# Optimization experiments

Measured on AMD Instinct MI355X. Metric: run time of the kernel, lower is better.

Reference implementation:

```python
import jax, jax.numpy as jnp
import numpy as np

N_NODES = 50000
N_EDGES = 1600000
N_GRAPHS = 512
IN_SIZE = 44
HIDDEN = 256
CONV_NUMS = 3


def setup_inputs() -> dict:
    key = jax.random.key(0)
    ks = jax.random.split(key, 10)
    h = jax.random.normal(ks[0], (N_NODES, IN_SIZE), dtype=jnp.float32)
    src = jax.random.randint(ks[1], (N_EDGES,), 0, N_NODES)
    dst = jax.random.randint(ks[2], (N_EDGES,), 0, N_NODES)
    graph_ids = jnp.sort(jax.random.randint(ks[3], (N_NODES,), 0, N_GRAPHS))
    # learned params (kaiming-ish scale)
    W_proj = jax.random.normal(ks[4], (IN_SIZE, HIDDEN), dtype=jnp.float32) * (2.0 / IN_SIZE) ** 0.5
    b_proj = jnp.zeros((HIDDEN,), dtype=jnp.float32)
    W_lin = jax.random.normal(ks[5], (HIDDEN, HIDDEN), dtype=jnp.float32) * (2.0 / HIDDEN) ** 0.5
    b_lin = jnp.zeros((HIDDEN,), dtype=jnp.float32)
    W_out = jax.random.normal(ks[6], (HIDDEN * CONV_NUMS, HIDDEN), dtype=jnp.float32) * (2.0 / (HIDDEN * CONV_NUMS)) ** 0.5
    b_out = jnp.zeros((HIDDEN,), dtype=jnp.float32)
    return {"h": h, "src": src, "dst": dst, "graph_ids": graph_ids,
            "W_proj": W_proj, "b_proj": b_proj, "W_lin": W_lin, "b_lin": b_lin,
            "W_out": W_out, "b_out": b_out}


def reference(h, src, dst, graph_ids, W_proj, b_proj, W_lin, b_lin, W_out, b_out):
    # initial projection
    h = h @ W_proj + b_proj  # [N, HIDDEN]
    # in-degree for mean aggregation (nodes with 0 in-edges get 0 aggregate)
    ones_e = jnp.ones((src.shape[0],), dtype=h.dtype)
    deg = jax.ops.segment_sum(ones_e, dst, num_segments=N_NODES)  # [N]
    inv_deg = jnp.where(deg > 0, 1.0 / jnp.maximum(deg, 1.0), 0.0)[:, None]
    outs = []
    for _ in range(CONV_NUMS):
        # DGL GINConv(mean, eps=0): h' = linear(h + mean_{u in N(v)} h_u)
        agg = jax.ops.segment_sum(h[src], dst, num_segments=N_NODES) * inv_deg
        h = (h + agg) @ W_lin + b_lin  # shared linear across layers
        outs.append(h)
    res = jnp.concatenate(outs, axis=1) @ W_out + b_out  # [N, HIDDEN]
    # dgl.mean_nodes: per-graph mean readout
    cnt = jax.ops.segment_sum(jnp.ones((N_NODES,), dtype=res.dtype), graph_ids, num_segments=N_GRAPHS)
    g_sum = jax.ops.segment_sum(res, graph_ids, num_segments=N_GRAPHS)
    return g_sum / jnp.maximum(cnt, 1.0)[:, None]
```

## Files before the change

kernel.cpp:

```cpp
#include <hip/hip_runtime.h>
#include <hip/hip_fp8.h>

#define N_NODES   50000
#define N_EDGES   1600000
#define N_GRAPHS  512
#define IN_SIZE   44
#define HIDDEN    256
#define CONV_NUMS 3
#define NBK       ((N_NODES + 255) / 256)
#define XK        48
#define XK8       64

typedef __attribute__((ext_vector_type(8))) short short8v;
typedef __attribute__((ext_vector_type(4))) float f32x4;
typedef __attribute__((ext_vector_type(2))) float f32x2;

__device__ __forceinline__ float bf2f(unsigned short u) {
    return __uint_as_float(((unsigned int)u) << 16);
}
__device__ __forceinline__ unsigned short f2bf(float f) {
    unsigned int u = __float_as_uint(f);
    unsigned int r = (u + 0x7fffu + ((u >> 16) & 1u)) >> 16;
    return (unsigned short)r;
}

#if __has_builtin(__builtin_amdgcn_cvt_f32_fp8)
template <int SEL>
__device__ __forceinline__ float fp8tof(unsigned int w) {
    return __builtin_amdgcn_cvt_f32_fp8((int)w, SEL);
}
#else
template <int SEL>
__device__ __forceinline__ float fp8tof(unsigned int w) {
    __hip_fp8_e4m3 q;
    q.__x = (__hip_fp8_storage_t)((w >> (SEL * 8)) & 0xff);
    return (float)q;
}
#endif

#if __has_builtin(__builtin_amdgcn_cvt_pk_f32_fp8)
template <int HI>
__device__ __forceinline__ f32x2 pk2f(unsigned int w) {
    return __builtin_amdgcn_cvt_pk_f32_fp8((int)w, HI != 0);
}
#else
template <int HI>
__device__ __forceinline__ f32x2 pk2f(unsigned int w) {
    f32x2 r;
    r.x = fp8tof<2 * HI>(w);
    r.y = fp8tof<2 * HI + 1>(w);
    return r;
}
#endif

#if __has_builtin(__builtin_amdgcn_cvt_pk_fp8_f32)
__device__ __forceinline__ unsigned int pk4fp8(float f0, float f1, float f2, float f3) {
    int lo = __builtin_amdgcn_cvt_pk_fp8_f32(f0, f1, 0, false);
    return (unsigned int)__builtin_amdgcn_cvt_pk_fp8_f32(f2, f3, lo, true);
}
#else
__device__ __forceinline__ unsigned int pk4fp8(float f0, float f1, float f2, float f3) {
    __hip_fp8_e4m3 a(f0), b(f1), c(f2), d(f3);
    return (unsigned int)a.__x | ((unsigned int)b.__x << 8) |
           ((unsigned int)c.__x << 16) | ((unsigned int)d.__x << 24);
}
#endif

__device__ __forceinline__ unsigned char f2fp8(float f) {
    return (unsigned char)(pk4fp8(f, 0.f, 0.f, 0.f) & 0xff);
}

__global__ __launch_bounds__(256) void k_build0(const int* __restrict__ dst,
                                                const int* __restrict__ gid,
                                                const float* __restrict__ Wl,
                                                const float* __restrict__ Wproj,
                                                const float* __restrict__ X,
                                                int* __restrict__ bucket_cnt,
                                                int* __restrict__ gcnt,
                                                unsigned short* __restrict__ WlPack,
                                                unsigned short* __restrict__ WprojPack,
                                                unsigned short* __restrict__ Xb,
                                                unsigned char* __restrict__ Xb8p) {
    int b = blockIdx.x;
    int tid = threadIdx.x;
    if (b < 512) {
        __shared__ int hb[NBK];
        __shared__ int hg[N_GRAPHS];
        for (int i = tid; i < NBK; i += 256) hb[i] = 0;
        for (int i = tid; i < N_GRAPHS; i += 256) hg[i] = 0;
        __syncthreads();
        int t = b * 256 + tid;
        int stride = 512 * 256;
        for (int e = t; e < N_EDGES; e += stride) atomicAdd(&hb[dst[e] >> 8], 1);
        for (int v = t; v < N_NODES; v += stride) atomicAdd(&hg[gid[v]], 1);
        __syncthreads();
        for (int i = tid; i < NBK; i += 256) if (hb[i]) atomicAdd(&bucket_cnt[i], hb[i]);
        for (int i = tid; i < N_GRAPHS; i += 256) if (hg[i]) atomicAdd(&gcnt[i], hg[i]);
    } else if (b < 544) {
        int i = (b - 512) * 256 + tid;
        int kg = i >> 8, n = i & 255;
        short8v v;
#pragma unroll
        for (int j = 0; j < 8; j++) v[j] = (short)f2bf(Wl[(kg * 8 + j) * HIDDEN + n]);
        *(short8v*)(WlPack + (size_t)(kg * 256 + n) * 8) = v;
    } else if (b < 552) {
        int i = (b - 544) * 256 + tid;
        int kg = i >> 8, n = i & 255;
        short8v v;
#pragma unroll
        for (int j = 0; j < 8; j++) {
            int k = kg * 8 + j;
            v[j] = (k < IN_SIZE) ? (short)f2bf(Wproj[k * HIDDEN + n]) : (short)0;
        }
        *(short8v*)(WprojPack + (size_t)(kg * 256 + n) * 8) = v;
    } else {
        const int TOT8 = N_NODES * XK8;
        int id0 = (b - 552) * 2048 + tid;
#pragma unroll
        for (int j = 0; j < 8; j++) {
            int id = id0 + j * 256;
            if (id < TOT8) {
                int row = id >> 6, c = id & 63;
                float val = (c < IN_SIZE) ? X[row * IN_SIZE + c] : 0.f;
                Xb8p[id] = f2fp8(val);
                if (c < XK) Xb[(size_t)row * XK + c] = f2bf(val);
            }
        }
    }
}

__global__ void k_bscan(const int* __restrict__ bucket_cnt, int* __restrict__ bucket_base,
                        int* __restrict__ bucket_cursor, int* __restrict__ row_ptr) {
    __shared__ int s[256];
    int t = threadIdx.x;
    int v = (t < NBK) ? bucket_cnt[t] : 0;
    s[t] = v;
    __syncthreads();
    for (int off = 1; off < 256; off <<= 1) {
        int a = (t >= off) ? s[t - off] : 0;
        __syncthreads();
        s[t] += a;
        __syncthreads();
    }
    if (t < NBK) {
        int base = s[t] - v;
        bucket_base[t] = base;
        bucket_cursor[t] = base;
    }
    if (t == 0) {
        bucket_base[NBK] = N_EDGES;
        row_ptr[N_NODES] = N_EDGES;
    }
}

#define BCH 8192
__global__ __launch_bounds__(256) void k_passB(const int* __restrict__ src,
                                               const int* __restrict__ dst,
                                               int* __restrict__ bucket_cursor,
                                               int* __restrict__ pairs) {
    __shared__ int hist[NBK];
    __shared__ int excl[NBK];
    __shared__ int cur[NBK];
    __shared__ int gbase[NBK];
    __shared__ int lp[BCH];
    __shared__ int sc[256];
    int tid = threadIdx.x;
    int e0 = blockIdx.x * BCH;
    int cnt = min(BCH, N_EDGES - e0);
    for (int i = tid; i < NBK; i += 256) hist[i] = 0;
    __syncthreads();
    for (int i = tid; i < cnt; i += 256) atomicAdd(&hist[dst[e0 + i] >> 8], 1);
    __syncthreads();
    int hv = (tid < NBK) ? hist[tid] : 0;
    sc[tid] = hv;
    __syncthreads();
    for (int off = 1; off < 256; off <<= 1) {
        int a = (tid >= off) ? sc[tid - off] : 0;
        __syncthreads();
        sc[tid] += a;
        __syncthreads();
    }
    if (tid < NBK) {
        excl[tid] = sc[tid] - hv;
        cur[tid]  = sc[tid] - hv;
    }
    __syncthreads();
    for (int i = tid; i < cnt; i += 256) {
        int d = dst[e0 + i];
        int b = d >> 8;
        int pos = atomicAdd(&cur[b], 1);
        lp[pos] = (b << 24) | ((d & 255) << 16) | src[e0 + i];
    }
    __syncthreads();
    if (tid < NBK && hist[tid] > 0)
        gbase[tid] = atomicAdd(&bucket_cursor[tid], hist[tid]);
    __syncthreads();
    for (int i = tid; i < cnt; i += 256) {
        int p = lp[i];
        int b = (p >> 24) & 0xff;
        pairs[gbase[b] + (i - excl[b])] = p;
    }
}

__global__ __launch_bounds__(256) void k_passC(const int* __restrict__ pairs,
                                               const int* __restrict__ bucket_base,
                                               int* __restrict__ row_ptr,
                                               unsigned short* __restrict__ colu) {
    __shared__ int hist[256];
    __shared__ int cur[256];
    __shared__ int sc[256];
    int b = blockIdx.x;
    int tid = threadIdx.x;
    int v0 = b << 8;
    int e0 = bucket_base[b], e1 = bucket_base[b + 1];
    hist[tid] = 0;
    __syncthreads();
    for (int i = e0 + tid; i < e1; i += 256) atomicAdd(&hist[(pairs[i] >> 16) & 0xff], 1);
    __syncthreads();
    int hv = hist[tid];
    sc[tid] = hv;
    __syncthreads();
    for (int off = 1; off < 256; off <<= 1) {
        int a = (tid >= off) ? sc[tid - off] : 0;
        __syncthreads();
        sc[tid] += a;
        __syncthreads();
    }
    int base = e0 + sc[tid] - hv;
    int v = v0 + tid;
    if (v < N_NODES) row_ptr[v] = base;
    cur[tid] = base;
    __syncthreads();
    for (int i = e0 + tid; i < e1; i += 256) {
        int p = pairs[i];
        int pos = atomicAdd(&cur[(p >> 16) & 0xff], 1);
        colu[pos] = (unsigned short)(p & 0xffff);
    }
}

#define TLS 264
#define K1S 72
__global__ __launch_bounds__(512, 8) void k_layer1(const unsigned short* __restrict__ Xb,
                                                   const unsigned char* __restrict__ Xb8p,
                                                   const int* __restrict__ row_ptr,
                                                   const unsigned short* __restrict__ colu,
                                                   const unsigned short* __restrict__ WprojPack,
                                                   const float* __restrict__ bp,
                                                   const unsigned short* __restrict__ WlPack,
                                                   const float* __restrict__ bl,
                                                   const int* __restrict__ gid,
                                                   unsigned short* __restrict__ hout,
                                                   unsigned char* __restrict__ hout8,
                                                   float* __restrict__ GsumL) {
    __shared__ unsigned short tl[64 * TLS];
    unsigned short* tl1 = tl;
    float* redbase = (float*)(tl + 64 * K1S);
    __shared__ float bpm[64];
    __shared__ int gl[64];
    int tid = threadIdx.x;
    int w = tid >> 6, lane = tid & 63, quad = lane >> 4, l16 = lane & 15;
    int g = lane >> 4, sub = lane & 15;
    int m0 = blockIdx.x * 64;
    float* red = redbase + w * 256;

    const unsigned int* X8 = (const unsigned int*)Xb8p;
    for (int rr = 0; rr < 8; rr++) {
        int r = w * 8 + rr;
        int v = m0 + r;
        f32x2 A = {0.f, 0.f};
        f32x2 Bv = {0.f, 0.f};
        int s = 0, e = 0;
        if (v < N_NODES) { s = row_ptr[v]; e = row_ptr[v + 1]; }
        int i = s;
        for (; i + 8 <= e; i += 8) {
            int ua = colu[i + g];
            int ub = colu[i + 4 + g];
            unsigned int pa = X8[ua * 16 + sub];
            unsigned int pb = X8[ub * 16 + sub];
            A  += pk2f<0>(pa) + pk2f<0>(pb);
            Bv += pk2f<1>(pa) + pk2f<1>(pb);
        }
        if (i + 4 <= e) {
            int ua = colu[i + g];
            unsigned int pa = X8[ua * 16 + sub];
            A += pk2f<0>(pa);
            Bv += pk2f<1>(pa);
            i += 4;
        }
        if (i + g < e) {
            int ua = colu[i + g];
            unsigned int pa = X8[ua * 16 + sub];
            A += pk2f<0>(pa);
            Bv += pk2f<1>(pa);
        }
        *(f32x4*)(red + g * 64 + sub * 4) = (f32x4){A.x, A.y, Bv.x, Bv.y};
        float ssum = (red[0 * 64 + lane] + red[1 * 64 + lane])
                   + (red[2 * 64 + lane] + red[3 * 64 + lane]);
        float val = 0.f;
        float mul = 1.f;
        if (v < N_NODES) {
            float inv = 0.f;
            if (e > s) { inv = 1.0f / (float)(e - s); mul = 2.f; }
            float self = (lane < XK) ? bf2f(Xb[(size_t)v * XK + lane]) : 0.f;
            val = self + inv * ssum;
        }
        tl1[r * K1S + lane] = (lane < XK) ? f2bf(val) : (unsigned short)0;
        if (lane == 0) bpm[r] = mul;
    }
    if (tid < 64) gl[tid] = (m0 + tid < N_NODES) ? gid[m0 + tid] : -1;
    __syncthreads();

    int n0 = w * 32;
    f32x4 acc[4][2];
#pragma unroll
    for (int mt = 0; mt < 4; mt++) {
        acc[mt][0] = (f32x4){0.f, 0.f, 0.f, 0.f};
        acc[mt][1] = (f32x4){0.f, 0.f, 0.f, 0.f};
    }
#pragma unroll
    for (int ks = 0; ks < 2; ks++) {
        int kg = ks * 4 + quad;
        short8v bfr0 = *(const short8v*)(WprojPack + (size_t)(kg * 256 + n0 + l16) * 8);
        short8v bfr1 = *(const short8v*)(WprojPack + (size_t)(kg * 256 + n0 + 16 + l16) * 8);
#pragma unroll
        for (int mt = 0; mt < 4; mt++) {
            short8v afr = *(const short8v*)(tl1 + (mt * 16 + l16) * K1S + ks * 32 + quad * 8);
            acc[mt][0] = __builtin_amdgcn_mfma_f32_16x16x32_bf16(afr, bfr0, acc[mt][0], 0, 0, 0);
            acc[mt][1] = __builtin_amdgcn_mfma_f32_16x16x32_bf16(afr, bfr1, acc[mt][1], 0, 0, 0);
        }
    }
    __syncthreads();
#pragma unroll
    for (int nt = 0; nt < 2; nt++) {
        int colg = n0 + nt * 16 + l16;
        float bb = bp[colg];
#pragma unroll
        for (int mt = 0; mt < 4; mt++)
#pragma unroll
            for (int r = 0; r < 4; r++) {
                int row = mt * 16 + quad * 4 + r;
                tl[row * TLS + colg] = f2bf(acc[mt][nt][r] + bb * bpm[row]);
            }
    }
    __syncthreads();

#pragma unroll
    for (int mt = 0; mt < 4; mt++) {
        acc[mt][0] = (f32x4){0.f, 0.f, 0.f, 0.f};
        acc[mt][1] = (f32x4){0.f, 0.f, 0.f, 0.f};
    }
#pragma unroll
    for (int ks = 0; ks < 8; ks++) {
        int kg = ks * 4 + quad;
        short8v bfr0 = *(const short8v*)(WlPack + (size_t)(kg * 256 + n0 + l16) * 8);
        short8v bfr1 = *(const short8v*)(WlPack + (size_t)(kg * 256 + n0 + 16 + l16) * 8);
#pragma unroll
        for (int mt = 0; mt < 4; mt++) {
            short8v afr = *(const short8v*)(tl + (mt * 16 + l16) * TLS + ks * 32 + quad * 8);
            acc[mt][0] = __builtin_amdgcn_mfma_f32_16x16x32_bf16(afr, bfr0, acc[mt][0], 0, 0, 0);
            acc[mt][1] = __builtin_amdgcn_mfma_f32_16x16x32_bf16(afr, bfr1, acc[mt][1], 0, 0, 0);
        }
    }
    __syncthreads();

#pragma unroll
    for (int nt = 0; nt < 2; nt++) {
        int colg = n0 + nt * 16 + l16;
        float bb = bl[colg];
#pragma unroll
        for (int mt = 0; mt < 4; mt++)
#pragma unroll
            for (int r = 0; r < 4; r++)
                tl[(mt * 16 + quad * 4 + r) * TLS + colg] = f2bf(acc[mt][nt][r] + bb);
    }
    __syncthreads();

    for (int i = tid; i < 64 * 64; i += 512) {
        int r = i >> 6, c4 = i & 63;
        int v = m0 + r;
        if (v < N_NODES) {
            ushort4 q = *(ushort4*)(tl + r * TLS + c4 * 4);
            ((ushort4*)hout)[(size_t)v * 64 + c4] = q;
            ((unsigned int*)hout8)[(size_t)v * 64 + c4] =
                pk4fp8(bf2f(q.x), bf2f(q.y), bf2f(q.z), bf2f(q.w));
        }
    }
    {
        int c = tid & 255;
        int r0 = (tid >> 8) * 32;
        float a2 = 0.f;
        int curg = gl[r0];
        for (int r = r0; r < r0 + 32; r++) {
            int gg = gl[r];
            if (gg < 0) break;
            if (gg != curg) {
                atomicAdd(&GsumL[curg * HIDDEN + c], a2);
                a2 = 0.f;
                curg = gg;
            }
            a2 += bf2f(tl[r * TLS + c]);
        }
        if (curg >= 0) atomicAdd(&GsumL[curg * HIDDEN + c], a2);
    }
}

__global__ __launch_bounds__(512, 8) void k_layer(const unsigned short* __restrict__ h,
                                                  const unsigned char* __restrict__ h8,
                                                  const int* __restrict__ row_ptr,
                                                  const unsigned short* __restrict__ colu,
                                                  const unsigned short* __restrict__ Wpack,
                                                  const float* __restrict__ bias,
                                                  const int* __restrict__ gid,
                                                  unsigned short* __restrict__ hout,
                                                  unsigned char* __restrict__ hout8,
                                                  int write8,
                                                  float* __restrict__ GsumL) {
    __shared__ unsigned short tl[64 * TLS];
    __shared__ int gl[64];
    int tid = threadIdx.x;
    int w = tid >> 6, lane = tid & 63, quad = lane >> 4, l16 = lane & 15;
    int m0 = blockIdx.x * 64;

    const unsigned int* h8v = (const unsigned int*)h8;
    const ushort4* hv = (const ushort4*)h;
    for (int rr = 0; rr < 8; rr++) {
        int r = w * 8 + rr;
        int v = m0 + r;
        f32x2 A = {0.f, 0.f};
        f32x2 B = {0.f, 0.f};
        if (v < N_NODES) {
            int s = row_ptr[v], e = row_ptr[v + 1];
            int i = s;
            for (; i + 8 <= e; i += 8) {
                int u0 = colu[i],     u1 = colu[i + 1];
                int u2 = colu[i + 2], u3 = colu[i + 3];
                int u4 = colu[i + 4], u5 = colu[i + 5];
                int u6 = colu[i + 6], u7 = colu[i + 7];
                unsigned int p0 = h8v[(size_t)u0 * 64 + lane];
                unsigned int p1 = h8v[(size_t)u1 * 64 + lane];
                unsigned int p2 = h8v[(size_t)u2 * 64 + lane];
                unsigned int p3 = h8v[(size_t)u3 * 64 + lane];
                unsigned int p4 = h8v[(size_t)u4 * 64 + lane];
                unsigned int p5 = h8v[(size_t)u5 * 64 + lane];
                unsigned int p6 = h8v[(size_t)u6 * 64 + lane];
                unsigned int p7 = h8v[(size_t)u7 * 64 + lane];
                A += (pk2f<0>(p0) + pk2f<0>(p1)) + (pk2f<0>(p2) + pk2f<0>(p3))
                   + (pk2f<0>(p4) + pk2f<0>(p5)) + (pk2f<0>(p6) + pk2f<0>(p7));
                B += (pk2f<1>(p0) + pk2f<1>(p1)) + (pk2f<1>(p2) + pk2f<1>(p3))
                   + (pk2f<1>(p4) + pk2f<1>(p5)) + (pk2f<1>(p6) + pk2f<1>(p7));
            }
            for (; i + 4 <= e; i += 4) {
                int u0 = colu[i], u1 = colu[i + 1], u2 = colu[i + 2], u3 = colu[i + 3];
                unsigned int p0 = h8v[(size_t)u0 * 64 + lane];
                unsigned int p1 = h8v[(size_t)u1 * 64 + lane];
                unsigned int p2 = h8v[(size_t)u2 * 64 + lane];
                unsigned int p3 = h8v[(size_t)u3 * 64 + lane];
                A += (pk2f<0>(p0) + pk2f<0>(p1)) + (pk2f<0>(p2) + pk2f<0>(p3));
                B += (pk2f<1>(p0) + pk2f<1>(p1)) + (pk2f<1>(p2) + pk2f<1>(p3));
            }
            for (; i < e; i++) {
                unsigned int p = h8v[(size_t)colu[i] * 64 + lane];
                A += pk2f<0>(p);
                B += pk2f<1>(p);
            }
            float inv = (e > s) ? 1.0f / (float)(e - s) : 0.0f;
            ushort4 hs = hv[(size_t)v * 64 + lane];
            A.x = bf2f(hs.x) + inv * A.x;
            A.y = bf2f(hs.y) + inv * A.y;
            B.x = bf2f(hs.z) + inv * B.x;
            B.y = bf2f(hs.w) + inv * B.y;
        }
        ushort4 o;
        o.x = f2bf(A.x); o.y = f2bf(A.y); o.z = f2bf(B.x); o.w = f2bf(B.y);
        *(ushort4*)(tl + r * TLS + lane * 4) = o;
    }
    if (tid < 64) gl[tid] = (m0 + tid < N_NODES) ? gid[m0 + tid] : -1;
    __syncthreads();

    int n0 = w * 32;
    f32x4 acc[4][2];
#pragma unroll
    for (int mt = 0; mt < 4; mt++) {
        acc[mt][0] = (f32x4){0.f, 0.f, 0.f, 0.f};
        acc[mt][1] = (f32x4){0.f, 0.f, 0.f, 0.f};
    }
#pragma unroll
    for (int ks = 0; ks < 8; ks++) {
        int kg = ks * 4 + quad;
        short8v bfr0 = *(const short8v*)(Wpack + (size_t)(kg * 256 + n0 + l16) * 8);
        short8v bfr1 = *(const short8v*)(Wpack + (size_t)(kg * 256 + n0 + 16 + l16) * 8);
#pragma unroll
        for (int mt = 0; mt < 4; mt++) {
            short8v afr = *(const short8v*)(tl + (mt * 16 + l16) * TLS + ks * 32 + quad * 8);
            acc[mt][0] = __builtin_amdgcn_mfma_f32_16x16x32_bf16(afr, bfr0, acc[mt][0], 0, 0, 0);
            acc[mt][1] = __builtin_amdgcn_mfma_f32_16x16x32_bf16(afr, bfr1, acc[mt][1], 0, 0, 0);
        }
    }
    __syncthreads();

#pragma unroll
    for (int nt = 0; nt < 2; nt++) {
        int colg = n0 + nt * 16 + l16;
        float bb = bias[colg];
#pragma unroll
        for (int mt = 0; mt < 4; mt++)
#pragma unroll
            for (int r = 0; r < 4; r++)
                tl[(mt * 16 + quad * 4 + r) * TLS + colg] = f2bf(acc[mt][nt][r] + bb);
    }
    __syncthreads();

    for (int i = tid; i < 64 * 64; i += 512) {
        int r = i >> 6, c4 = i & 63;
        int v = m0 + r;
        if (v < N_NODES) {
            ushort4 q = *(ushort4*)(tl + r * TLS + c4 * 4);
            ((ushort4*)hout)[(size_t)v * 64 + c4] = q;
            if (write8)
                ((unsigned int*)hout8)[(size_t)v * 64 + c4] =
                    pk4fp8(bf2f(q.x), bf2f(q.y), bf2f(q.z), bf2f(q.w));
        }
    }
    {
        int c = tid & 255;
        int r0 = (tid >> 8) * 32;
        float a2 = 0.f;
        int curg = gl[r0];
        for (int r = r0; r < r0 + 32; r++) {
            int g = gl[r];
            if (g < 0) break;
            if (g != curg) {
                atomicAdd(&GsumL[curg * HIDDEN + c], a2);
                a2 = 0.f;
                curg = g;
            }
            a2 += bf2f(tl[r * TLS + c]);
        }
        if (curg >= 0) atomicAdd(&GsumL[curg * HIDDEN + c], a2);
    }
}

__global__ __launch_bounds__(256) void k_out(const float* __restrict__ Gsum,
                                             const int* __restrict__ gcnt,
                                             const float* __restrict__ Wout,
                                             const float* __restrict__ bout,
                                             float* __restrict__ out) {
    int g = blockIdx.x;
    int c = threadIdx.x;
    __shared__ float gm[HIDDEN * CONV_NUMS];
    float invc = 1.0f / fmaxf((float)gcnt[g], 1.0f);
    for (int i = c; i < HIDDEN * CONV_NUMS; i += 256) {
        int l = i >> 8;
        int k = i & 255;
        gm[i] = Gsum[(size_t)l * N_GRAPHS * HIDDEN + g * HIDDEN + k] * invc;
    }
    __syncthreads();
    float acc = bout[c];
    const float4* gm4 = (const float4*)gm;
    for (int k0 = 0; k0 < HIDDEN * CONV_NUMS; k0 += 4) {
        float4 gv = gm4[k0 >> 2];
        acc += gv.x * Wout[(k0 + 0) * HIDDEN + c];
        acc += gv.y * Wout[(k0 + 1) * HIDDEN + c];
        acc += gv.z * Wout[(k0 + 2) * HIDDEN + c];
        acc += gv.w * Wout[(k0 + 3) * HIDDEN + c];
    }
    out[g * HIDDEN + c] = acc;
}

extern "C" void kernel_launch(void* const* d_in, const int* in_sizes, int n_in,
                              void* d_out, int out_size, void* d_ws, size_t ws_size,
                              hipStream_t stream) {
    const float* X    = (const float*)d_in[0];
    const int*   src  = (const int*)d_in[1];
    const int*   dst  = (const int*)d_in[2];
    const int*   gid  = (const int*)d_in[3];
    const float* Wp   = (const float*)d_in[4];
    const float* bp   = (const float*)d_in[5];
    const float* Wl   = (const float*)d_in[6];
    const float* bl   = (const float*)d_in[7];
    const float* Wout = (const float*)d_in[8];
    const float* bout = (const float*)d_in[9];
    float* out = (float*)d_out;

    char* ws = (char*)d_ws;
    size_t off = 0;
    auto alloc = [&](size_t bytes) {
        char* p = ws + off;
        off += (bytes + 255) & ~size_t(255);
        return p;
    };
    unsigned short* h         = (unsigned short*)alloc(sizeof(short) * N_NODES * HIDDEN);
    unsigned short* t         = (unsigned short*)alloc(sizeof(short) * N_NODES * HIDDEN);
    unsigned char*  h8a       = (unsigned char*)alloc((size_t)N_NODES * HIDDEN);
    unsigned char*  h8b       = (unsigned char*)alloc((size_t)N_NODES * HIDDEN);
    unsigned short* WlPack    = (unsigned short*)alloc(sizeof(short) * HIDDEN * HIDDEN);
    unsigned short* WprojPack = (unsigned short*)alloc(sizeof(short) * 8 * 256 * 8);
    unsigned short* Xb        = (unsigned short*)alloc(sizeof(short) * N_NODES * XK);
    unsigned char*  Xb8p      = (unsigned char*)alloc((size_t)N_NODES * XK8);
    int*   pairs   = (int*)alloc(sizeof(int) * N_EDGES);
    unsigned short* colu = (unsigned short*)alloc(sizeof(short) * N_EDGES);
    int*   row_ptr = (int*)alloc(sizeof(int) * (N_NODES + 1));
    int*   bucket_base   = (int*)alloc(sizeof(int) * (NBK + 1));
    int*   bucket_cursor = (int*)alloc(sizeof(int) * NBK);
    char*  zero0 = ws + off;
    int*   bucket_cnt = (int*)alloc(sizeof(int) * NBK);
    int*   gcnt       = (int*)alloc(sizeof(int) * N_GRAPHS);
    float* Gsum       = (float*)alloc(sizeof(float) * CONV_NUMS * N_GRAPHS * HIDDEN);
    size_t zero_bytes = (size_t)((char*)(Gsum + CONV_NUMS * N_GRAPHS * HIDDEN) - zero0);

    hipMemsetAsync(zero0, 0, zero_bytes, stream);

    {
        const int TOT8 = N_NODES * XK8;
        int ncast = (TOT8 + 2047) / 2048;
        k_build0<<<552 + ncast, 256, 0, stream>>>(dst, gid, Wl, Wp, X, bucket_cnt,
                                                  gcnt, WlPack, WprojPack, Xb, Xb8p);
    }
    k_bscan<<<1, 256, 0, stream>>>(bucket_cnt, bucket_base, bucket_cursor, row_ptr);
    k_passB<<<(N_EDGES + BCH - 1) / BCH, 256, 0, stream>>>(src, dst, bucket_cursor, pairs);
    k_passC<<<NBK, 256, 0, stream>>>(pairs, bucket_base, row_ptr, colu);

    k_layer1<<<(N_NODES + 63) / 64, 512, 0, stream>>>(
        Xb, Xb8p, row_ptr, colu, WprojPack, bp, WlPack, bl, gid, h, h8a, Gsum);

    k_layer<<<(N_NODES + 63) / 64, 512, 0, stream>>>(
        h, h8a, row_ptr, colu, WlPack, bl, gid, t, h8b, 1,
        Gsum + (size_t)1 * N_GRAPHS * HIDDEN);

    k_layer<<<(N_NODES + 63) / 64, 512, 0, stream>>>(
        t, h8b, row_ptr, colu, WlPack, bl, gid, h, h8a, 0,
        Gsum + (size_t)2 * N_GRAPHS * HIDDEN);

    k_out<<<N_GRAPHS, 256, 0, stream>>>(Gsum, gcnt, Wout, bout, out);
}
```

Measured before the change: 362.3 us.

## Split FP8 node features into column planes for cache-friendly gather

Stores the FP8 copy of hidden features as four 64-byte column planes instead of one 256-byte row per node. The layer kernel now gathers one plane at a time, with each wave splitting lanes into 4 edge groups of 16 columns and combining them through shuffle reductions. The intent is to shrink the working set per pass so gathered rows stay in L2/MALL across the plane passes. The cost is four passes over the CSR indices and extra shuffles per node. The tail-edge handling also becomes branch-free, using a clamped index and a 0/1 mask.

```diff
diff --git a/kernel.cpp b/kernel.cpp
--- a/kernel.cpp
+++ b/kernel.cpp
@@ -10,6 +10,7 @@
 #define NBK       ((N_NODES + 255) / 256)
 #define XK        48
 #define XK8       64
+#define PLANE_U   ((size_t)N_NODES * 16)
 
 typedef __attribute__((ext_vector_type(8))) short short8v;
 typedef __attribute__((ext_vector_type(4))) float f32x4;
@@ -287,11 +288,15 @@
             Bv += pk2f<1>(pa);
             i += 4;
         }
-        if (i + g < e) {
-            int ua = colu[i + g];
+        if (i < e) {
+            int idx = i + g;
+            int cl = (idx < e) ? idx : (e - 1);
+            int ua = colu[cl];
             unsigned int pa = X8[ua * 16 + sub];
-            A += pk2f<0>(pa);
-            Bv += pk2f<1>(pa);
+            float mvalid = (idx < e) ? 1.f : 0.f;
+            f32x2 za = pk2f<0>(pa), zb = pk2f<1>(pa);
+            A.x += mvalid * za.x; A.y += mvalid * za.y;
+            Bv.x += mvalid * zb.x; Bv.y += mvalid * zb.y;
         }
         *(f32x4*)(red + g * 64 + sub * 4) = (f32x4){A.x, A.y, Bv.x, Bv.y};
         float ssum = (red[0 * 64 + lane] + red[1 * 64 + lane])
@@ -381,7 +386,7 @@
         if (v < N_NODES) {
             ushort4 q = *(ushort4*)(tl + r * TLS + c4 * 4);
             ((ushort4*)hout)[(size_t)v * 64 + c4] = q;
-            ((unsigned int*)hout8)[(size_t)v * 64 + c4] =
+            ((unsigned int*)hout8)[(size_t)(c4 >> 4) * PLANE_U + (size_t)v * 16 + (c4 & 15)] =
                 pk4fp8(bf2f(q.x), bf2f(q.y), bf2f(q.z), bf2f(q.w));
         }
     }
@@ -419,60 +424,64 @@
     __shared__ int gl[64];
     int tid = threadIdx.x;
     int w = tid >> 6, lane = tid & 63, quad = lane >> 4, l16 = lane & 15;
+    int g = lane & 3, sub = lane >> 2;
     int m0 = blockIdx.x * 64;
 
     const unsigned int* h8v = (const unsigned int*)h8;
     const ushort4* hv = (const ushort4*)h;
-    for (int rr = 0; rr < 8; rr++) {
-        int r = w * 8 + rr;
-        int v = m0 + r;
-        f32x2 A = {0.f, 0.f};
-        f32x2 B = {0.f, 0.f};
-        if (v < N_NODES) {
-            int s = row_ptr[v], e = row_ptr[v + 1];
+
+    for (int p = 0; p < 4; p++) {
+        const unsigned int* plane = h8v + (size_t)p * PLANE_U;
+        for (int rr = 0; rr < 8; rr++) {
+            int r = w * 8 + rr;
+            int v = m0 + r;
+            f32x2 A = {0.f, 0.f};
+            f32x2 B = {0.f, 0.f};
+            int s = 0, e = 0;
+            if (v < N_NODES) { s = row_ptr[v]; e = row_ptr[v + 1]; }
             int i = s;
             for (; i + 8 <= e; i += 8) {
-                int u0 = colu[i],     u1 = colu[i + 1];
-                int u2 = colu[i + 2], u3 = colu[i + 3];
-                int u4 = colu[i + 4], u5 = colu[i + 5];
-                int u6 = colu[i + 6], u7 = colu[i + 7];
-                unsigned int p0 = h8v[(size_t)u0 * 64 + lane];
-                unsigned int p1 = h8v[(size_t)u1 * 64 + lane];
-                unsigned int p2 = h8v[(size_t)u2 * 64 + lane];
-                unsigned int p3 = h8v[(size_t)u3 * 64 + lane];
-                unsigned int p4 = h8v[(size_t)u4 * 64 + lane];
-                unsigned int p5 = h8v[(size_t)u5 * 64 + lane];
-                unsigned int p6 = h8v[(size_t)u6 * 64 + lane];
-                unsigned int p7 = h8v[(size_t)u7 * 64 + lane];
-                A += (pk2f<0>(p0) + pk2f<0>(p1)) + (pk2f<0>(p2) + pk2f<0>(p3))
-                   + (pk2f<0>(p4) + pk2f<0>(p5)) + (pk2f<0>(p6) + pk2f<0>(p7));
-                B += (pk2f<1>(p0) + pk2f<1>(p1)) + (pk2f<1>(p2) + pk2f<1>(p3))
-                   + (pk2f<1>(p4) + pk2f<1>(p5)) + (pk2f<1>(p6) + pk2f<1>(p7));
-            }
-            for (; i + 4 <= e; i += 4) {
-                int u0 = colu[i], u1 = colu[i + 1], u2 = colu[i + 2], u3 = colu[i + 3];
-                unsigned int p0 = h8v[(size_t)u0 * 64 + lane];
-                unsigned int p1 = h8v[(size_t)u1 * 64 + lane];
-                unsigned int p2 = h8v[(size_t)u2 * 64 + lane];
-                unsigned int p3 = h8v[(size_t)u3 * 64 + lane];
-                A += (pk2f<0>(p0) + pk2f<0>(p1)) + (pk2f<0>(p2) + pk2f<0>(p3));
-                B += (pk2f<1>(p0) + pk2f<1>(p1)) + (pk2f<1>(p2) + pk2f<1>(p3));
-            }
-            for (; i < e; i++) {
-                unsigned int p = h8v[(size_t)colu[i] * 64 + lane];
-                A += pk2f<0>(p);
-                B += pk2f<1>(p);
-            }
-            float inv = (e > s) ? 1.0f / (float)(e - s) : 0.0f;
-            ushort4 hs = hv[(size_t)v * 64 + lane];
-            A.x = bf2f(hs.x) + inv * A.x;
-            A.y = bf2f(hs.y) + inv * A.y;
-            B.x = bf2f(hs.z) + inv * B.x;
-            B.y = bf2f(hs.w) + inv * B.y;
-        }
-        ushort4 o;
-        o.x = f2bf(A.x); o.y = f2bf(A.y); o.z = f2bf(B.x); o.w = f2bf(B.y);
-        *(ushort4*)(tl + r * TLS + lane * 4) = o;
+                int ua = colu[i + g];
+                int ub = colu[i + 4 + g];
+                unsigned int pa = plane[(size_t)ua * 16 + sub];
+                unsigned int pb = plane[(size_t)ub * 16 + sub];
+                A += pk2f<0>(pa) + pk2f<0>(pb);
+                B += pk2f<1>(pa) + pk2f<1>(pb);
+            }
+            if (i + 4 <= e) {
+                int ua = colu[i + g];
+                unsigned int pa = plane[(size_t)ua * 16 + sub];
+                A += pk2f<0>(pa);
+                B += pk2f<1>(pa);
+                i += 4;
+            }
+            if (i < e) {
+                int idx = i + g;
+                int cl = (idx < e) ? idx : (e - 1);
+                int ua = colu[cl];
+                unsigned int pa = plane[(size_t)ua * 16 + sub];
+                float mvalid = (idx < e) ? 1.f : 0.f;
+                f32x2 za = pk2f<0>(pa), zb = pk2f<1>(pa);
+                A.x += mvalid * za.x; A.y += mvalid * za.y;
+                B.x += mvalid * zb.x; B.y += mvalid * zb.y;
+            }
+            A.x += __shfl_xor(A.x, 1); A.y += __shfl_xor(A.y, 1);
+            B.x += __shfl_xor(B.x, 1); B.y += __shfl_xor(B.y, 1);
+            A.x += __shfl_xor(A.x, 2); A.y += __shfl_xor(A.y, 2);
+            B.x += __shfl_xor(B.x, 2); B.y += __shfl_xor(B.y, 2);
+            if (g == 0) {
+                ushort4 o = {0, 0, 0, 0};
+                if (v < N_NODES) {
+                    float inv = (e > s) ? 1.0f / (float)(e - s) : 0.0f;
+                    ushort4 hs = hv[(size_t)v * 64 + p * 16 + sub];
+                    o.x = f2bf(bf2f(hs.x) + inv * A.x);
+                    o.y = f2bf(bf2f(hs.y) + inv * A.y);
+                    o.z = f2bf(bf2f(hs.z) + inv * B.x);
+                    o.w = f2bf(bf2f(hs.w) + inv * B.y);
+                }
+                *(ushort4*)(tl + r * TLS + p * 64 + sub * 4) = o;
+            }
+        }
     }
     if (tid < 64) gl[tid] = (m0 + tid < N_NODES) ? gid[m0 + tid] : -1;
     __syncthreads();
@@ -517,7 +526,7 @@
             ushort4 q = *(ushort4*)(tl + r * TLS + c4 * 4);
             ((ushort4*)hout)[(size_t)v * 64 + c4] = q;
             if (write8)
-                ((unsigned int*)hout8)[(size_t)v * 64 + c4] =
+                ((unsigned int*)hout8)[(size_t)(c4 >> 4) * PLANE_U + (size_t)v * 16 + (c4 & 15)] =
                     pk4fp8(bf2f(q.x), bf2f(q.y), bf2f(q.z), bf2f(q.w));
         }
     }
@@ -527,12 +536,12 @@
         float a2 = 0.f;
         int curg = gl[r0];
         for (int r = r0; r < r0 + 32; r++) {
-            int g = gl[r];
-            if (g < 0) break;
-            if (g != curg) {
+            int gg = gl[r];
+            if (gg < 0) break;
+            if (gg != curg) {
                 atomicAdd(&GsumL[curg * HIDDEN + c], a2);
                 a2 = 0.f;
-                curg = g;
+                curg = gg;
             }
             a2 += bf2f(tl[r * TLS + c]);
         }
```

After: 523.1 us. 44.4% more time.
